# Kernel tuning notes

Measured on AMD Instinct MI355X. Metric: run time of the kernel, lower is better.

## Reference

```python
import jax, jax.numpy as jnp
import numpy as np

N = 50000      # num nodes
E = 800000     # num edges
IN = 128       # in_channels
OUT = 128      # out_channels
H = 8          # num_heads
HD = OUT // H  # out_channels_conv (per-head dim)
EDIM = 16      # edge_dim
HID = 512      # hidden_dim of dst MLP


def layer_norm(x, w, b, eps=1e-5):
    m = jnp.mean(x, axis=-1, keepdims=True)
    v = jnp.var(x, axis=-1, keepdims=True)
    return (x - m) * jax.lax.rsqrt(v + eps) * w + b


def setup_inputs() -> dict:
    key = jax.random.key(0)
    ks = jax.random.split(key, 16)
    lin = lambda k, i, o: jax.random.normal(k, (i, o), jnp.float32) / np.sqrt(i)
    return {
        "x": jax.random.normal(ks[0], (N, IN), jnp.float32),
        "edge_attr": jax.random.normal(ks[1], (E, EDIM), jnp.float32),
        "edge_index": jax.random.randint(ks[2], (2, E), 0, N),
        "Wq": lin(ks[3], IN, OUT), "bq": jnp.zeros((OUT,), jnp.float32),
        "Wk": lin(ks[4], IN, OUT), "bk": jnp.zeros((OUT,), jnp.float32),
        "Wv": lin(ks[5], IN, OUT), "bv": jnp.zeros((OUT,), jnp.float32),
        "Ws": lin(ks[6], IN, OUT), "bs": jnp.zeros((OUT,), jnp.float32),
        "We": lin(ks[7], EDIM, OUT), "be": jnp.zeros((OUT,), jnp.float32),
        "Wp": lin(ks[8], OUT, OUT), "bp": jnp.zeros((OUT,), jnp.float32),
        "ln_a_w": jnp.ones((IN,), jnp.float32), "ln_a_b": jnp.zeros((IN,), jnp.float32),
        "ln_m_w": jnp.ones((OUT,), jnp.float32), "ln_m_b": jnp.zeros((OUT,), jnp.float32),
        "W1": lin(ks[9], OUT, HID), "b1": jnp.zeros((HID,), jnp.float32),
        "W2": lin(ks[10], HID, OUT), "b2": jnp.zeros((OUT,), jnp.float32),
    }


def reference(x, edge_attr, edge_index, Wq, bq, Wk, bk, Wv, bv, Ws, bs, We, be,
              Wp, bp, ln_a_w, ln_a_b, ln_m_w, ln_m_b, W1, b1, W2, b2):
    src, dst = edge_index[0], edge_index[1]

    x_skip = x
    xn = layer_norm(x, ln_a_w, ln_a_b)           # pre-attention LN
    x_r = xn @ Ws + bs                           # lin_self

    q = (xn @ Wq + bq).reshape(N, H, HD)
    k = (xn @ Wk + bk).reshape(N, H, HD)
    v = (xn @ Wv + bv).reshape(N, H, HD)
    e = (edge_attr @ We + be).reshape(E, H, HD)

    # edge-indexed attention: score(edge) = <q[dst], k[src]+e> / sqrt(HD)
    kj = k[src] + e                                              # [E,H,HD]
    scores = jnp.einsum('ehd,ehd->eh', q[dst], kj) / np.sqrt(HD)  # [E,H]

    # segment softmax over incoming edges of each dst node
    smax = jax.ops.segment_max(scores, dst, num_segments=N)     # [N,H]
    smax = jnp.where(jnp.isfinite(smax), smax, 0.0)             # guard empty segments
    ex = jnp.exp(scores - smax[dst])                            # [E,H]
    denom = jax.ops.segment_sum(ex, dst, num_segments=N)        # [N,H]
    alpha = ex / jnp.maximum(denom[dst], 1e-16)                 # [E,H]

    msg = (v[src] + e) * alpha[..., None]                       # [E,H,HD]
    out = jax.ops.segment_sum(msg, dst, num_segments=N).reshape(N, OUT)

    out = (out + x_r) @ Wp + bp                                 # projection
    out = out + x_skip                                          # residual

    # dst-node MLP with pre-LN and residual
    h = layer_norm(out, ln_m_w, ln_m_b)
    nodes_new = jax.nn.gelu(h @ W1 + b1) @ W2 + b2 + out
    return nodes_new, edge_attr
```

## Files before the change

### kernel.cpp

```cpp
#include <hip/hip_runtime.h>
#include <math.h>

#define N_NODES 50000
#define N_EDGES 800000

typedef __attribute__((ext_vector_type(8))) short bf16x8;
typedef __attribute__((ext_vector_type(4))) float f32x4;

__device__ __forceinline__ short f2bf(float f){
  unsigned u = __float_as_uint(f);
  unsigned r = (u + 0x7FFFu + ((u >> 16) & 1u)) >> 16;
  return (short)r;
}
__device__ __forceinline__ unsigned pkbf(float lo, float hi){
  return (unsigned)(unsigned short)f2bf(lo) | ((unsigned)(unsigned short)f2bf(hi) << 16);
}

__device__ __forceinline__ float gelu_f(float x){
  float z = 0.7978845608028654f*(x + 0.044715f*x*x*x);
  float e = __expf(2.0f*z);
  return 0.5f*x*(2.0f - 2.0f/(e + 1.0f));
}

#define BF_LO(u) __uint_as_float((u)<<16)
#define BF_HI(u) __uint_as_float((u)&0xffff0000u)

__global__ __launch_bounds__(256) void k_tconv(const float* __restrict__ W, short* __restrict__ Wt,
                                               int K, int Nn){
  int i = blockIdx.x*256 + threadIdx.x;
  if (i < K*Nn){
    int n = i / K, k = i - n*K;
    Wt[(size_t)n*K + k] = f2bf(W[(size_t)k*Nn + n]);
  }
}

struct TC6 { const float* src[6]; short* dst[6]; };
__global__ __launch_bounds__(256) void k_tconv6(TC6 t){
  int b = blockIdx.y;
  const float* W = t.src[b];
  short* Wt = t.dst[b];
  int i = blockIdx.x*256 + threadIdx.x;
  int n = i >> 7, k = i & 127;
  Wt[n*128 + k] = f2bf(W[k*128 + n]);
}

__global__ __launch_bounds__(256) void k_wqm(const float* __restrict__ Wq, const float* __restrict__ We,
                                             const float* __restrict__ bq,
                                             float* __restrict__ Wqm, float* __restrict__ bqm){
  int i = blockIdx.x*256 + threadIdx.x;
  if (i < 16384){
    int k = i >> 7, j = i & 127;
    int h = j >> 4, c = j & 15;
    float s = 0.f;
    #pragma unroll
    for (int dd = 0; dd < 16; ++dd)
      s += Wq[k*128 + h*16 + dd] * We[c*128 + h*16 + dd];
    Wqm[i] = s;
    if (k == 0){
      float t = 0.f;
      #pragma unroll
      for (int dd = 0; dd < 16; ++dd)
        t += bq[h*16 + dd] * We[c*128 + h*16 + dd];
      bqm[j] = t;
    }
  }
}

__global__ __launch_bounds__(256) void k_deg(const int* __restrict__ dst, int* __restrict__ deg){
  int i = blockIdx.x*256 + threadIdx.x;
  if (i < N_EDGES) atomicAdd(&deg[dst[i]], 1);
}

__global__ __launch_bounds__(256) void k_bsum(const int* __restrict__ deg,
                                              int* __restrict__ bsum, int* __restrict__ hist){
  __shared__ int lhist[64];
  __shared__ int wred[4];
  int tid = threadIdx.x;
  int i = blockIdx.x*256 + tid;
  if (tid < 64) lhist[tid] = 0;
  __syncthreads();
  int v = (i < N_NODES) ? deg[i] : 0;
  if (i < N_NODES) atomicAdd(&lhist[v > 63 ? 63 : v], 1);
  int s = v;
  #pragma unroll
  for (int sh = 32; sh >= 1; sh >>= 1) s += __shfl_xor(s, sh, 64);
  if ((tid & 63) == 0) wred[tid >> 6] = s;
  __syncthreads();
  if (tid == 0) bsum[blockIdx.x] = wred[0] + wred[1] + wred[2] + wred[3];
  if (tid < 64){ int c = lhist[tid]; if (c) atomicAdd(&hist[tid], c); }
}

__global__ __launch_bounds__(256) void k_bscan(const int* __restrict__ bsum, int* __restrict__ bbase,
                                               const int* __restrict__ hist, int* __restrict__ histcur){
  __shared__ int wsum[4];
  int tid = threadIdx.x;
  int v = (tid < 196) ? bsum[tid] : 0;
  int incl = v;
  #pragma unroll
  for (int s = 1; s < 64; s <<= 1){
    int t = __shfl_up(incl, s, 64);
    if ((tid & 63) >= s) incl += t;
  }
  if ((tid & 63) == 63) wsum[tid >> 6] = incl;
  __syncthreads();
  if (tid == 0){ int c = 0; for (int j = 0; j < 4; ++j){ int t = wsum[j]; wsum[j] = c; c += t; } }
  __syncthreads();
  if (tid < 196) bbase[tid] = wsum[tid >> 6] + (incl - v);
  if (tid < 64){
    int h = hist[tid];
    int inc = h;
    #pragma unroll
    for (int s = 1; s < 64; s <<= 1){
      int t = __shfl_up(inc, s, 64);
      if (tid >= s) inc += t;
    }
    int total = __shfl(inc, 63, 64);
    histcur[tid] = total - inc;
  }
}

__global__ __launch_bounds__(256) void k_apply(const int* __restrict__ deg, const int* __restrict__ bbase,
                                               int* __restrict__ off, int* __restrict__ cursor){
  __shared__ int wsum[4];
  int tid = threadIdx.x;
  int i = blockIdx.x*256 + tid;
  int v = (i < N_NODES) ? deg[i] : 0;
  int incl = v;
  #pragma unroll
  for (int s = 1; s < 64; s <<= 1){
    int t = __shfl_up(incl, s, 64);
    if ((tid & 63) >= s) incl += t;
  }
  if ((tid & 63) == 63) wsum[tid >> 6] = incl;
  __syncthreads();
  if (tid == 0){ int c = 0; for (int j = 0; j < 4; ++j){ int t = wsum[j]; wsum[j] = c; c += t; } }
  __syncthreads();
  int excl = bbase[blockIdx.x] + wsum[tid >> 6] + (incl - v);
  if (i < N_NODES){
    off[i] = excl; cursor[i] = excl;
    if (i == N_NODES-1) off[N_NODES] = excl + v;
  }
}

__global__ __launch_bounds__(256) void k_scatter(const int* __restrict__ dst, const int* __restrict__ src,
                                                 const float* __restrict__ edge_attr,
                                                 int* __restrict__ cursor,
                                                 int* __restrict__ esrc, ushort* __restrict__ eab){
  int i = blockIdx.x*256 + threadIdx.x;
  if (i < N_EDGES){
    int d = dst[i];
    int pos = atomicAdd(&cursor[d], 1);
    esrc[pos] = src[i];
    const float* ea = edge_attr + (size_t)i*16;
    float4 a = *(const float4*)(ea+0), b = *(const float4*)(ea+4),
           c = *(const float4*)(ea+8), e = *(const float4*)(ea+12);
    uint4 o0, o1;
    o0.x = pkbf(a.x,a.y); o0.y = pkbf(a.z,a.w); o0.z = pkbf(b.x,b.y); o0.w = pkbf(b.z,b.w);
    o1.x = pkbf(c.x,c.y); o1.y = pkbf(c.z,c.w); o1.z = pkbf(e.x,e.y); o1.w = pkbf(e.z,e.w);
    *(uint4*)&eab[(size_t)pos*16]     = o0;
    *(uint4*)&eab[(size_t)pos*16 + 8] = o1;
  }
}

__global__ __launch_bounds__(256) void k_perm(const int* __restrict__ deg, const int* __restrict__ off,
                                              int* __restrict__ histcur,
                                              int* __restrict__ perm, int2* __restrict__ rng){
  __shared__ int lhist[64];
  __shared__ int lbase[64];
  int tid = threadIdx.x;
  int i = blockIdx.x*256 + tid;
  if (tid < 64) lhist[tid] = 0;
  __syncthreads();
  int d = 0, b = 0, loc = 0;
  bool ok = i < N_NODES;
  if (ok){
    d = deg[i];
    b = d > 63 ? 63 : d;
    loc = atomicAdd(&lhist[b], 1);
  }
  __syncthreads();
  if (tid < 64){
    int c = lhist[tid];
    lbase[tid] = c ? atomicAdd(&histcur[tid], c) : 0;
  }
  __syncthreads();
  if (ok){
    int pos = lbase[b] + loc;
    perm[pos] = i;
    int o = off[i];
    rng[pos] = make_int2(o, o + d);
  }
}

__global__ __launch_bounds__(256) void k_nodeproj(
  const float* __restrict__ x, const float* __restrict__ lnw, const float* __restrict__ lnb,
  const short* __restrict__ Wtq, const short* __restrict__ Wtqm,
  const short* __restrict__ Wtk, const short* __restrict__ Wtv, const short* __restrict__ Wts,
  const float* __restrict__ bq, const float* __restrict__ bqm,
  const float* __restrict__ bk, const float* __restrict__ bv, const float* __restrict__ bs,
  ushort* __restrict__ qb, ushort* __restrict__ qweb,
  ushort* __restrict__ kb, ushort* __restrict__ vb, float* __restrict__ xr)
{
  __shared__ short A[64][136];
  int tid = threadIdx.x;
  int rbase = blockIdx.x * 64;

  {
    int r = tid >> 2, j = tid & 3;
    int row = rbase + r;
    bool ok = row < N_NODES;
    const float* xp = x + (size_t)row*128 + j*32;
    float vals[32];
    #pragma unroll
    for (int i = 0; i < 8; ++i){
      float4 t = ok ? *(const float4*)(xp + i*4) : make_float4(0,0,0,0);
      vals[i*4+0]=t.x; vals[i*4+1]=t.y; vals[i*4+2]=t.z; vals[i*4+3]=t.w;
    }
    float s = 0.f, s2 = 0.f;
    #pragma unroll
    for (int i = 0; i < 32; ++i){ s += vals[i]; s2 += vals[i]*vals[i]; }
    s  += __shfl_xor(s, 1, 64);  s  += __shfl_xor(s, 2, 64);
    s2 += __shfl_xor(s2, 1, 64); s2 += __shfl_xor(s2, 2, 64);
    float mean = s * 0.0078125f;
    float var  = s2 * 0.0078125f - mean*mean;
    float rstd = rsqrtf(var + 1e-5f);
    #pragma unroll
    for (int i = 0; i < 32; ++i){
      int col = j*32 + i;
      float xn = (vals[i]-mean)*rstd*lnw[col] + lnb[col];
      A[r][col] = f2bf(xn);
    }
  }
  __syncthreads();

  int lane = tid & 63, wave = tid >> 6;
  int row16 = lane & 15, kg = lane >> 4;
  int cb = wave * 32;

  auto gemm = [&](const short* __restrict__ B, const float* __restrict__ bias,
                  float* __restrict__ Of, ushort* __restrict__ Ob){
    f32x4 acc[4][2] = {};
    #pragma unroll
    for (int kk = 0; kk < 128; kk += 32){
      int k0 = kk + kg*8;
      bf16x8 a0 = *(const bf16x8*)&A[ 0 + row16][k0];
      bf16x8 a1 = *(const bf16x8*)&A[16 + row16][k0];
      bf16x8 a2 = *(const bf16x8*)&A[32 + row16][k0];
      bf16x8 a3 = *(const bf16x8*)&A[48 + row16][k0];
      bf16x8 b0 = *(const bf16x8*)&B[(size_t)(cb +      row16)*128 + k0];
      bf16x8 b1 = *(const bf16x8*)&B[(size_t)(cb + 16 + row16)*128 + k0];
      acc[0][0] = __builtin_amdgcn_mfma_f32_16x16x32_bf16(a0, b0, acc[0][0], 0,0,0);
      acc[1][0] = __builtin_amdgcn_mfma_f32_16x16x32_bf16(a1, b0, acc[1][0], 0,0,0);
      acc[2][0] = __builtin_amdgcn_mfma_f32_16x16x32_bf16(a2, b0, acc[2][0], 0,0,0);
      acc[3][0] = __builtin_amdgcn_mfma_f32_16x16x32_bf16(a3, b0, acc[3][0], 0,0,0);
      acc[0][1] = __builtin_amdgcn_mfma_f32_16x16x32_bf16(a0, b1, acc[0][1], 0,0,0);
      acc[1][1] = __builtin_amdgcn_mfma_f32_16x16x32_bf16(a1, b1, acc[1][1], 0,0,0);
      acc[2][1] = __builtin_amdgcn_mfma_f32_16x16x32_bf16(a2, b1, acc[2][1], 0,0,0);
      acc[3][1] = __builtin_amdgcn_mfma_f32_16x16x32_bf16(a3, b1, acc[3][1], 0,0,0);
    }
    float bv0 = bias[cb + row16], bv1 = bias[cb + 16 + row16];
    #pragma unroll
    for (int rt = 0; rt < 4; ++rt){
      #pragma unroll
      for (int i = 0; i < 4; ++i){
        int row = rbase + rt*16 + kg*4 + i;
        if (row < N_NODES){
          float v0 = acc[rt][0][i] + bv0;
          float v1 = acc[rt][1][i] + bv1;
          if (Of){
            Of[(size_t)row*128 + cb      + row16] = v0;
            Of[(size_t)row*128 + cb + 16 + row16] = v1;
          } else {
            Ob[(size_t)row*128 + cb      + row16] = (ushort)f2bf(v0);
            Ob[(size_t)row*128 + cb + 16 + row16] = (ushort)f2bf(v1);
          }
        }
      }
    }
  };
  gemm(Wtq,  bq,  nullptr, qb);
  gemm(Wtqm, bqm, nullptr, qweb);
  gemm(Wtk,  bk,  nullptr, kb);
  gemm(Wtv,  bv,  nullptr, vb);
  gemm(Wts,  bs,  xr,  nullptr);
}

__global__ __launch_bounds__(256) void k_agg(
  const ushort* __restrict__ qb, const ushort* __restrict__ qweb,
  const ushort* __restrict__ kbf, const ushort* __restrict__ vbf,
  const ushort* __restrict__ eab, const float* __restrict__ We, const float* __restrict__ be,
  const int* __restrict__ esrc, const int* __restrict__ perm, const int2* __restrict__ rng,
  float* __restrict__ xr)
{
  int tid = threadIdx.x;
  int gid = blockIdx.x*8 + (tid >> 5);
  int node = perm[gid];
  int2 r = rng[gid];
  int beg = r.x, end = r.y;
  int l = tid & 31;
  int d0 = l*4;
  int h  = l >> 2;
  int c0 = (l & 3)*4;

  uint2 qw = *(const uint2*)&qb[(size_t)node*128 + d0];
  float4 qv = make_float4(BF_LO(qw.x), BF_HI(qw.x), BF_LO(qw.y), BF_HI(qw.y));
  uint2 qew = *(const uint2*)&qweb[(size_t)node*128 + h*16 + c0];
  float4 qe = make_float4(BF_LO(qew.x), BF_HI(qew.x), BF_LO(qew.y), BF_HI(qew.y));
  float m = -INFINITY, den = 0.f;
  float4 va = make_float4(0,0,0,0);
  float4 S  = make_float4(0,0,0,0);

  int p = beg;

#define AGG_STEP(J)                                                            \
  {                                                                            \
    int sidx[J];                                                               \
    _Pragma("unroll")                                                          \
    for (int j = 0; j < J; ++j) sidx[j] = esrc[p+j];                           \
    uint2 kw[J], vw[J], ew[J];                                                 \
    _Pragma("unroll")                                                          \
    for (int j = 0; j < J; ++j){                                               \
      kw[j] = *(const uint2*)&kbf[(size_t)sidx[j]*128 + d0];                   \
      vw[j] = *(const uint2*)&vbf[(size_t)sidx[j]*128 + d0];                   \
      ew[j] = *(const uint2*)&eab[(size_t)(p+j)*16 + c0];                      \
    }                                                                          \
    float sc[J];                                                               \
    _Pragma("unroll")                                                          \
    for (int j = 0; j < J; ++j){                                               \
      float pp = qv.x*BF_LO(kw[j].x) + qv.y*BF_HI(kw[j].x)                     \
               + qv.z*BF_LO(kw[j].y) + qv.w*BF_HI(kw[j].y)                     \
               + qe.x*BF_LO(ew[j].x) + qe.y*BF_HI(ew[j].x)                     \
               + qe.z*BF_LO(ew[j].y) + qe.w*BF_HI(ew[j].y);                    \
      pp += __shfl_xor(pp,1,64); pp += __shfl_xor(pp,2,64);                    \
      sc[j] = pp*0.25f;                                                        \
    }                                                                          \
    float mn = m;                                                              \
    _Pragma("unroll")                                                          \
    for (int j = 0; j < J; ++j) mn = fmaxf(mn, sc[j]);                         \
    float corr = __expf(m - mn);                                               \
    float w[J]; float ds = 0.f;                                                \
    _Pragma("unroll")                                                          \
    for (int j = 0; j < J; ++j){ w[j] = __expf(sc[j]-mn); ds += w[j]; }        \
    den = den*corr + ds;                                                       \
    float ax=0.f, ay=0.f, az=0.f, aw2=0.f, sx=0.f, sy=0.f, sz=0.f, sw=0.f;     \
    _Pragma("unroll")                                                          \
    for (int j = 0; j < J; ++j){                                               \
      ax += w[j]*BF_LO(vw[j].x); ay += w[j]*BF_HI(vw[j].x);                    \
      az += w[j]*BF_LO(vw[j].y); aw2+= w[j]*BF_HI(vw[j].y);                    \
      sx += w[j]*BF_LO(ew[j].x); sy += w[j]*BF_HI(ew[j].x);                    \
      sz += w[j]*BF_LO(ew[j].y); sw += w[j]*BF_HI(ew[j].y);                    \
    }                                                                          \
    va.x = va.x*corr + ax; va.y = va.y*corr + ay;                              \
    va.z = va.z*corr + az; va.w = va.w*corr + aw2;                             \
    S.x  = S.x *corr + sx; S.y  = S.y *corr + sy;                              \
    S.z  = S.z *corr + sz; S.w  = S.w *corr + sw;                              \
    m = mn;                                                                    \
  }

  for (; p + 8 <= end; p += 8) AGG_STEP(8)
  for (; p + 4 <= end; p += 4) AGG_STEP(4)
  for (; p < end; ++p){
    int s = esrc[p];
    uint2 kw = *(const uint2*)&kbf[(size_t)s*128 + d0];
    uint2 vw = *(const uint2*)&vbf[(size_t)s*128 + d0];
    uint2 ew = *(const uint2*)&eab[(size_t)p*16 + c0];
    float pp = qv.x*BF_LO(kw.x) + qv.y*BF_HI(kw.x)
             + qv.z*BF_LO(kw.y) + qv.w*BF_HI(kw.y)
             + qe.x*BF_LO(ew.x) + qe.y*BF_HI(ew.x)
             + qe.z*BF_LO(ew.y) + qe.w*BF_HI(ew.y);
    pp += __shfl_xor(pp,1,64); pp += __shfl_xor(pp,2,64);
    float sc = pp*0.25f;
    float mn = fmaxf(m, sc);
    float corr = __expf(m - mn);
    float pe = __expf(sc - mn);
    den = den*corr + pe;
    va.x = va.x*corr + pe*BF_LO(vw.x);
    va.y = va.y*corr + pe*BF_HI(vw.x);
    va.z = va.z*corr + pe*BF_LO(vw.y);
    va.w = va.w*corr + pe*BF_HI(vw.y);
    S.x = S.x*corr + pe*BF_LO(ew.x);
    S.y = S.y*corr + pe*BF_HI(ew.x);
    S.z = S.z*corr + pe*BF_LO(ew.y);
    S.w = S.w*corr + pe*BF_HI(ew.y);
    m = mn;
  }

  if (end > beg){
    float inv = 1.0f/den;
    float4 acc = va;
    int gb = (tid & 63) & 60;
    #pragma unroll
    for (int g = 0; g < 4; ++g){
      float s0 = __shfl(S.x, gb+g, 64);
      float s1 = __shfl(S.y, gb+g, 64);
      float s2 = __shfl(S.z, gb+g, 64);
      float s3 = __shfl(S.w, gb+g, 64);
      float4 w0 = *(const float4*)&We[(g*4+0)*128 + d0];
      float4 w1 = *(const float4*)&We[(g*4+1)*128 + d0];
      float4 w2 = *(const float4*)&We[(g*4+2)*128 + d0];
      float4 w3 = *(const float4*)&We[(g*4+3)*128 + d0];
      acc.x += s0*w0.x + s1*w1.x + s2*w2.x + s3*w3.x;
      acc.y += s0*w0.y + s1*w1.y + s2*w2.y + s3*w3.y;
      acc.z += s0*w0.z + s1*w1.z + s2*w2.z + s3*w3.z;
      acc.w += s0*w0.w + s1*w1.w + s2*w2.w + s3*w3.w;
    }
    float4 bev = *(const float4*)&be[d0];
    float4 xv = *(const float4*)&xr[(size_t)node*128 + d0];
    xv.x += acc.x*inv + bev.x;
    xv.y += acc.y*inv + bev.y;
    xv.z += acc.z*inv + bev.z;
    xv.w += acc.w*inv + bev.w;
    *(float4*)&xr[(size_t)node*128 + d0] = xv;
  }
}

__global__ __launch_bounds__(256) void k_post(
  const float* __restrict__ aggout, const float* __restrict__ x,
  const short* __restrict__ Wtp, const float* __restrict__ bp,
  const float* __restrict__ lnw, const float* __restrict__ lnb,
  float* __restrict__ res, short* __restrict__ A2)
{
  __shared__ short A[64][136];
  __shared__ float rf[64][132];
  int tid = threadIdx.x;
  int rbase = blockIdx.x * 64;

  {
    int r = tid >> 2, j = tid & 3;
    int row = rbase + r;
    const float* p = aggout + (size_t)row*128 + j*32;
    #pragma unroll
    for (int i = 0; i < 8; ++i){
      float4 t = *(const float4*)(p + i*4);
      int c = j*32 + i*4;
      A[r][c+0] = f2bf(t.x); A[r][c+1] = f2bf(t.y);
      A[r][c+2] = f2bf(t.z); A[r][c+3] = f2bf(t.w);
    }
  }
  __syncthreads();

  int lane = tid & 63, wave = tid >> 6;
  int row16 = lane & 15, kg = lane >> 4;
  int cb = wave * 32;

  f32x4 acc[4][2] = {};
  #pragma unroll
  for (int kk = 0; kk < 128; kk += 32){
    int k0 = kk + kg*8;
    bf16x8 a0 = *(const bf16x8*)&A[ 0 + row16][k0];
    bf16x8 a1 = *(const bf16x8*)&A[16 + row16][k0];
    bf16x8 a2 = *(const bf16x8*)&A[32 + row16][k0];
    bf16x8 a3 = *(const bf16x8*)&A[48 + row16][k0];
    bf16x8 b0 = *(const bf16x8*)&Wtp[(size_t)(cb +      row16)*128 + k0];
    bf16x8 b1 = *(const bf16x8*)&Wtp[(size_t)(cb + 16 + row16)*128 + k0];
    acc[0][0] = __builtin_amdgcn_mfma_f32_16x16x32_bf16(a0, b0, acc[0][0], 0,0,0);
    acc[1][0] = __builtin_amdgcn_mfma_f32_16x16x32_bf16(a1, b0, acc[1][0], 0,0,0);
    acc[2][0] = __builtin_amdgcn_mfma_f32_16x16x32_bf16(a2, b0, acc[2][0], 0,0,0);
    acc[3][0] = __builtin_amdgcn_mfma_f32_16x16x32_bf16(a3, b0, acc[3][0], 0,0,0);
    acc[0][1] = __builtin_amdgcn_mfma_f32_16x16x32_bf16(a0, b1, acc[0][1], 0,0,0);
    acc[1][1] = __builtin_amdgcn_mfma_f32_16x16x32_bf16(a1, b1, acc[1][1], 0,0,0);
    acc[2][1] = __builtin_amdgcn_mfma_f32_16x16x32_bf16(a2, b1, acc[2][1], 0,0,0);
    acc[3][1] = __builtin_amdgcn_mfma_f32_16x16x32_bf16(a3, b1, acc[3][1], 0,0,0);
  }
  float bv0 = bp[cb + row16], bv1 = bp[cb + 16 + row16];
  #pragma unroll
  for (int rt = 0; rt < 4; ++rt){
    #pragma unroll
    for (int i = 0; i < 4; ++i){
      int rl = rt*16 + kg*4 + i;
      int row = rbase + rl;
      float v0 = acc[rt][0][i] + bv0;
      float v1 = acc[rt][1][i] + bv1;
      if (row < N_NODES){
        v0 += x[(size_t)row*128 + cb      + row16];
        v1 += x[(size_t)row*128 + cb + 16 + row16];
        res[(size_t)row*128 + cb      + row16] = v0;
        res[(size_t)row*128 + cb + 16 + row16] = v1;
      }
      rf[rl][cb      + row16] = v0;
      rf[rl][cb + 16 + row16] = v1;
    }
  }
  __syncthreads();

  {
    int r = tid >> 2, j = tid & 3;
    int row = rbase + r;
    float vals[32];
    #pragma unroll
    for (int i = 0; i < 8; ++i){
      float4 t = *(const float4*)&rf[r][j*32 + i*4];
      vals[i*4+0]=t.x; vals[i*4+1]=t.y; vals[i*4+2]=t.z; vals[i*4+3]=t.w;
    }
    float s = 0.f, s2 = 0.f;
    #pragma unroll
    for (int i = 0; i < 32; ++i){ s += vals[i]; s2 += vals[i]*vals[i]; }
    s  += __shfl_xor(s, 1, 64);  s  += __shfl_xor(s, 2, 64);
    s2 += __shfl_xor(s2, 1, 64); s2 += __shfl_xor(s2, 2, 64);
    float mean = s * 0.0078125f;
    float var  = s2 * 0.0078125f - mean*mean;
    float rstd = rsqrtf(var + 1e-5f);
    #pragma unroll
    for (int i = 0; i < 32; ++i){
      int col = j*32 + i;
      float xn = (vals[i]-mean)*rstd*lnw[col] + lnb[col];
      A2[(size_t)row*128 + col] = f2bf(xn);
    }
  }
}

__global__ __launch_bounds__(256) void k_mlp1(
  const short* __restrict__ A2, const short* __restrict__ W1t, const float* __restrict__ b1,
  short* __restrict__ hid)
{
  __shared__ short A[64][136];
  int tid = threadIdx.x;
  int rbase = blockIdx.x * 64;
  int ch = blockIdx.y;
  for (int idx = tid; idx < 1024; idx += 256){
    int r = idx >> 4, g = idx & 15;
    *(uint4*)&A[r][g*8] = *(const uint4*)&A2[((size_t)(rbase + r))*128 + g*8];
  }
  __syncthreads();

  int lane = tid & 63, wave = tid >> 6;
  int row16 = lane & 15, kg = lane >> 4;
  int cb = ch*256 + wave*64;

  f32x4 acc[4][4] = {};
  #pragma unroll
  for (int kk = 0; kk < 128; kk += 32){
    int k0 = kk + kg*8;
    bf16x8 a[4], b[4];
    #pragma unroll
    for (int rt = 0; rt < 4; ++rt) a[rt] = *(const bf16x8*)&A[rt*16 + row16][k0];
    #pragma unroll
    for (int ct = 0; ct < 4; ++ct) b[ct] = *(const bf16x8*)&W1t[(size_t)(cb + ct*16 + row16)*128 + k0];
    #pragma unroll
    for (int rt = 0; rt < 4; ++rt)
      #pragma unroll
      for (int ct = 0; ct < 4; ++ct)
        acc[rt][ct] = __builtin_amdgcn_mfma_f32_16x16x32_bf16(a[rt], b[ct], acc[rt][ct], 0,0,0);
  }
  float bv[4];
  #pragma unroll
  for (int ct = 0; ct < 4; ++ct) bv[ct] = b1[cb + ct*16 + row16];
  #pragma unroll
  for (int rt = 0; rt < 4; ++rt){
    #pragma unroll
    for (int ct = 0; ct < 4; ++ct){
      #pragma unroll
      for (int i = 0; i < 4; ++i){
        int row = rbase + rt*16 + kg*4 + i;
        hid[(size_t)row*512 + cb + ct*16 + row16] = f2bf(gelu_f(acc[rt][ct][i] + bv[ct]));
      }
    }
  }
}

__global__ __launch_bounds__(256) void k_mlp2(
  const short* __restrict__ hid, const short* __restrict__ W2t, const float* __restrict__ b2,
  const float* __restrict__ res, float* __restrict__ out)
{
  __shared__ short A[64][136];
  int tid = threadIdx.x;
  int rbase = blockIdx.x * 64;
  int lane = tid & 63, wave = tid >> 6;
  int row16 = lane & 15, kg = lane >> 4;
  int cb = wave * 32;

  f32x4 acc[4][2] = {};
  for (int kc = 0; kc < 4; ++kc){
    __syncthreads();
    for (int idx = tid; idx < 1024; idx += 256){
      int r = idx >> 4, g = idx & 15;
      *(uint4*)&A[r][g*8] = *(const uint4*)&hid[((size_t)(rbase + r))*512 + kc*128 + g*8];
    }
    __syncthreads();
    #pragma unroll
    for (int kk = 0; kk < 128; kk += 32){
      int k0 = kk + kg*8;
      bf16x8 a0 = *(const bf16x8*)&A[ 0 + row16][k0];
      bf16x8 a1 = *(const bf16x8*)&A[16 + row16][k0];
      bf16x8 a2 = *(const bf16x8*)&A[32 + row16][k0];
      bf16x8 a3 = *(const bf16x8*)&A[48 + row16][k0];
      bf16x8 b0 = *(const bf16x8*)&W2t[(size_t)(cb +      row16)*512 + kc*128 + k0];
      bf16x8 b1 = *(const bf16x8*)&W2t[(size_t)(cb + 16 + row16)*512 + kc*128 + k0];
      acc[0][0] = __builtin_amdgcn_mfma_f32_16x16x32_bf16(a0, b0, acc[0][0], 0,0,0);
      acc[1][0] = __builtin_amdgcn_mfma_f32_16x16x32_bf16(a1, b0, acc[1][0], 0,0,0);
      acc[2][0] = __builtin_amdgcn_mfma_f32_16x16x32_bf16(a2, b0, acc[2][0], 0,0,0);
      acc[3][0] = __builtin_amdgcn_mfma_f32_16x16x32_bf16(a3, b0, acc[3][0], 0,0,0);
      acc[0][1] = __builtin_amdgcn_mfma_f32_16x16x32_bf16(a0, b1, acc[0][1], 0,0,0);
      acc[1][1] = __builtin_amdgcn_mfma_f32_16x16x32_bf16(a1, b1, acc[1][1], 0,0,0);
      acc[2][1] = __builtin_amdgcn_mfma_f32_16x16x32_bf16(a2, b1, acc[2][1], 0,0,0);
      acc[3][1] = __builtin_amdgcn_mfma_f32_16x16x32_bf16(a3, b1, acc[3][1], 0,0,0);
    }
  }
  float bv0 = b2[cb + row16], bv1 = b2[cb + 16 + row16];
  #pragma unroll
  for (int rt = 0; rt < 4; ++rt){
    #pragma unroll
    for (int i = 0; i < 4; ++i){
      int row = rbase + rt*16 + kg*4 + i;
      if (row < N_NODES){
        out[(size_t)row*128 + cb      + row16] = acc[rt][0][i] + bv0 + res[(size_t)row*128 + cb      + row16];
        out[(size_t)row*128 + cb + 16 + row16] = acc[rt][1][i] + bv1 + res[(size_t)row*128 + cb + 16 + row16];
      }
    }
  }
}

extern "C" void kernel_launch(void* const* d_in, const int* in_sizes, int n_in,
                              void* d_out, int out_size, void* d_ws, size_t ws_size,
                              hipStream_t stream)
{
  const float* x        = (const float*)d_in[0];
  const float* edge_attr= (const float*)d_in[1];
  const int*   edge_index=(const int*)d_in[2];
  const float* Wq = (const float*)d_in[3];  const float* bq = (const float*)d_in[4];
  const float* Wk = (const float*)d_in[5];  const float* bk = (const float*)d_in[6];
  const float* Wv = (const float*)d_in[7];  const float* bv = (const float*)d_in[8];
  const float* Wss= (const float*)d_in[9];  const float* bss= (const float*)d_in[10];
  const float* We = (const float*)d_in[11]; const float* be = (const float*)d_in[12];
  const float* Wp = (const float*)d_in[13]; const float* bp = (const float*)d_in[14];
  const float* lnaw=(const float*)d_in[15]; const float* lnab=(const float*)d_in[16];
  const float* lnmw=(const float*)d_in[17]; const float* lnmb=(const float*)d_in[18];
  const float* W1 = (const float*)d_in[19]; const float* b1 = (const float*)d_in[20];
  const float* W2 = (const float*)d_in[21]; const float* b2 = (const float*)d_in[22];

  float* ws = (float*)d_ws;
  const size_t NP128 = 6406144;
  const size_t NPH   = 3203072;
  ushort* qb   = (ushort*)ws;
  ushort* qweb = (ushort*)(ws + NPH);
  ushort* kbf  = (ushort*)(ws + 2*NPH);
  ushort* vbf  = (ushort*)(ws + 3*NPH);
  float*  xr   = ws + 4*NPH;
  float*  res  = ws + 4*NPH + NP128;
  ushort* eab  = (ushort*)res;
  short* wts   = (short*)(ws + 25624576);
  short* Wtq   = wts;
  short* Wtk   = wts + 16384;
  short* Wtv   = wts + 32768;
  short* Wts_  = wts + 49152;
  short* Wtp   = wts + 65536;
  short* Wtqm  = wts + 81920;
  short* W1t   = wts + 98304;
  short* W2t   = wts + 163840;
  float* Wqm_f = ws + 25624576 + 114688;
  float* bqm   = Wqm_f + 16384;
  int*   iw    = (int*)(bqm + 128);
  int* deg     = iw;
  int* hist    = iw + 50000;
  int* histcur = iw + 50064;
  int* bsum    = iw + 50128;
  int* bbase   = iw + 50324;
  int* off     = iw + 50520;
  int* cursor  = iw + 100521;
  int* perm    = iw + 150521;
  int2* rng    = (int2*)(iw + 200522);
  int* esrc    = iw + 300522;

  short* A2   = (short*)qb;
  short* hid  = (short*)qweb;

  const int* srcIdx = edge_index;
  const int* dstIdx = edge_index + N_EDGES;

  k_wqm<<<64, 256, 0, stream>>>(Wq, We, bq, Wqm_f, bqm);
  TC6 tc;
  tc.src[0]=Wq; tc.src[1]=Wk; tc.src[2]=Wv; tc.src[3]=Wss; tc.src[4]=Wp; tc.src[5]=Wqm_f;
  tc.dst[0]=Wtq; tc.dst[1]=Wtk; tc.dst[2]=Wtv; tc.dst[3]=Wts_; tc.dst[4]=Wtp; tc.dst[5]=Wtqm;
  k_tconv6<<<dim3(64,6), 256, 0, stream>>>(tc);
  k_tconv<<<256, 256, 0, stream>>>(W1, W1t, 128, 512);
  k_tconv<<<256, 256, 0, stream>>>(W2, W2t, 512, 128);

  hipMemsetAsync(deg, 0, 50064*sizeof(int), stream);
  k_deg<<<(N_EDGES+255)/256, 256, 0, stream>>>(dstIdx, deg);
  k_bsum<<<196, 256, 0, stream>>>(deg, bsum, hist);
  k_bscan<<<1, 256, 0, stream>>>(bsum, bbase, hist, histcur);
  k_apply<<<196, 256, 0, stream>>>(deg, bbase, off, cursor);
  k_scatter<<<(N_EDGES+255)/256, 256, 0, stream>>>(dstIdx, srcIdx, edge_attr, cursor, esrc, eab);
  k_perm<<<(N_NODES+255)/256, 256, 0, stream>>>(deg, off, histcur, perm, rng);

  k_nodeproj<<<782, 256, 0, stream>>>(x, lnaw, lnab, Wtq, Wtqm, Wtk, Wtv, Wts_,
                                      bq, bqm, bk, bv, bss, qb, qweb, kbf, vbf, xr);
  k_agg<<<N_NODES/8, 256, 0, stream>>>(qb, qweb, kbf, vbf, eab, We, be,
                                       esrc, perm, rng, xr);
  k_post<<<782, 256, 0, stream>>>(xr, x, Wtp, bp, lnmw, lnmb, res, A2);
  k_mlp1<<<dim3(782,2), 256, 0, stream>>>(A2, W1t, b1, hid);
  k_mlp2<<<782, 256, 0, stream>>>(hid, W2t, b2, res, (float*)d_out);

  hipMemcpyAsync((float*)d_out + (size_t)N_NODES*128, edge_attr,
                 (size_t)N_EDGES*16*sizeof(float), hipMemcpyDeviceToDevice, stream);
}
```

Before: 367.4 us.

## Merge weight prep kernels, fuse edge_attr copy into scatter, prefetch edge indices in aggregation

```diff
diff --git a/kernel.cpp b/kernel.cpp
--- a/kernel.cpp
+++ b/kernel.cpp
@@ -25,44 +25,44 @@
 #define BF_LO(u) __uint_as_float((u)<<16)
 #define BF_HI(u) __uint_as_float((u)&0xffff0000u)
 
-__global__ __launch_bounds__(256) void k_tconv(const float* __restrict__ W, short* __restrict__ Wt,
-                                               int K, int Nn){
-  int i = blockIdx.x*256 + threadIdx.x;
-  if (i < K*Nn){
-    int n = i / K, k = i - n*K;
-    Wt[(size_t)n*K + k] = f2bf(W[(size_t)k*Nn + n]);
-  }
-}
-
-struct TC6 { const float* src[6]; short* dst[6]; };
-__global__ __launch_bounds__(256) void k_tconv6(TC6 t){
-  int b = blockIdx.y;
-  const float* W = t.src[b];
-  short* Wt = t.dst[b];
-  int i = blockIdx.x*256 + threadIdx.x;
-  int n = i >> 7, k = i & 127;
-  Wt[n*128 + k] = f2bf(W[k*128 + n]);
-}
-
-__global__ __launch_bounds__(256) void k_wqm(const float* __restrict__ Wq, const float* __restrict__ We,
-                                             const float* __restrict__ bq,
-                                             float* __restrict__ Wqm, float* __restrict__ bqm){
-  int i = blockIdx.x*256 + threadIdx.x;
-  if (i < 16384){
+struct Prep {
+  const float* src[5]; short* dst[5];
+  const float* Wq; const float* We; const float* bq;
+  short* Wtqm; float* bqm;
+  const float* W1; short* W1t;
+  const float* W2; short* W2t;
+};
+__global__ __launch_bounds__(256) void k_prep(Prep a){
+  int blk = blockIdx.x, tid = threadIdx.x;
+  if (blk < 320){
+    int b = blk >> 6;
+    int i = (blk & 63)*256 + tid;
+    int n = i >> 7, k = i & 127;
+    a.dst[b][n*128 + k] = f2bf(a.src[b][k*128 + n]);
+  } else if (blk < 384){
+    int i = (blk - 320)*256 + tid;
     int k = i >> 7, j = i & 127;
     int h = j >> 4, c = j & 15;
     float s = 0.f;
     #pragma unroll
     for (int dd = 0; dd < 16; ++dd)
-      s += Wq[k*128 + h*16 + dd] * We[c*128 + h*16 + dd];
-    Wqm[i] = s;
+      s += a.Wq[k*128 + h*16 + dd] * a.We[c*128 + h*16 + dd];
+    a.Wtqm[j*128 + k] = f2bf(s);
     if (k == 0){
       float t = 0.f;
       #pragma unroll
       for (int dd = 0; dd < 16; ++dd)
-        t += bq[h*16 + dd] * We[c*128 + h*16 + dd];
-      bqm[j] = t;
-    }
+        t += a.bq[h*16 + dd] * a.We[c*128 + h*16 + dd];
+      a.bqm[j] = t;
+    }
+  } else if (blk < 640){
+    int i = (blk - 384)*256 + tid;
+    int n = i >> 7, k = i & 127;
+    a.W1t[n*128 + k] = f2bf(a.W1[k*512 + n]);
+  } else {
+    int i = (blk - 640)*256 + tid;
+    int n = i >> 9, k = i & 511;
+    a.W2t[n*512 + k] = f2bf(a.W2[k*128 + n]);
   }
 }
 
@@ -145,7 +145,8 @@
 __global__ __launch_bounds__(256) void k_scatter(const int* __restrict__ dst, const int* __restrict__ src,
                                                  const float* __restrict__ edge_attr,
                                                  int* __restrict__ cursor,
-                                                 int* __restrict__ esrc, ushort* __restrict__ eab){
+                                                 int* __restrict__ esrc, ushort* __restrict__ eab,
+                                                 float* __restrict__ eout){
   int i = blockIdx.x*256 + threadIdx.x;
   if (i < N_EDGES){
     int d = dst[i];
@@ -159,6 +160,11 @@
     o1.x = pkbf(c.x,c.y); o1.y = pkbf(c.z,c.w); o1.z = pkbf(e.x,e.y); o1.w = pkbf(e.z,e.w);
     *(uint4*)&eab[(size_t)pos*16]     = o0;
     *(uint4*)&eab[(size_t)pos*16 + 8] = o1;
+    float* op = eout + (size_t)i*16;
+    *(float4*)(op+0)  = a;
+    *(float4*)(op+4)  = b;
+    *(float4*)(op+8)  = c;
+    *(float4*)(op+12) = e;
   }
 }
 
@@ -311,6 +317,59 @@
   float4 S  = make_float4(0,0,0,0);
 
   int p = beg;
+
+  int s8[8];
+  {
+    bool have = (beg + 8 <= end);
+    #pragma unroll
+    for (int j = 0; j < 8; ++j) s8[j] = have ? esrc[beg + j] : 0;
+  }
+  for (; p + 8 <= end; p += 8){
+    int n8[8];
+    bool more = (p + 16 <= end);
+    #pragma unroll
+    for (int j = 0; j < 8; ++j) n8[j] = more ? esrc[p + 8 + j] : 0;
+    uint2 kw[8], vw[8], ew[8];
+    #pragma unroll
+    for (int j = 0; j < 8; ++j){
+      kw[j] = *(const uint2*)&kbf[(size_t)s8[j]*128 + d0];
+      vw[j] = *(const uint2*)&vbf[(size_t)s8[j]*128 + d0];
+      ew[j] = *(const uint2*)&eab[(size_t)(p+j)*16 + c0];
+    }
+    float sc[8];
+    #pragma unroll
+    for (int j = 0; j < 8; ++j){
+      float pp = qv.x*BF_LO(kw[j].x) + qv.y*BF_HI(kw[j].x)
+               + qv.z*BF_LO(kw[j].y) + qv.w*BF_HI(kw[j].y)
+               + qe.x*BF_LO(ew[j].x) + qe.y*BF_HI(ew[j].x)
+               + qe.z*BF_LO(ew[j].y) + qe.w*BF_HI(ew[j].y);
+      pp += __shfl_xor(pp,1,64); pp += __shfl_xor(pp,2,64);
+      sc[j] = pp*0.25f;
+    }
+    float mn = m;
+    #pragma unroll
+    for (int j = 0; j < 8; ++j) mn = fmaxf(mn, sc[j]);
+    float corr = __expf(m - mn);
+    float w[8]; float ds = 0.f;
+    #pragma unroll
+    for (int j = 0; j < 8; ++j){ w[j] = __expf(sc[j]-mn); ds += w[j]; }
+    den = den*corr + ds;
+    float ax=0.f, ay=0.f, az=0.f, aw2=0.f, sx=0.f, sy=0.f, sz=0.f, sw=0.f;
+    #pragma unroll
+    for (int j = 0; j < 8; ++j){
+      ax += w[j]*BF_LO(vw[j].x); ay += w[j]*BF_HI(vw[j].x);
+      az += w[j]*BF_LO(vw[j].y); aw2+= w[j]*BF_HI(vw[j].y);
+      sx += w[j]*BF_LO(ew[j].x); sy += w[j]*BF_HI(ew[j].x);
+      sz += w[j]*BF_LO(ew[j].y); sw += w[j]*BF_HI(ew[j].y);
+    }
+    va.x = va.x*corr + ax; va.y = va.y*corr + ay;
+    va.z = va.z*corr + az; va.w = va.w*corr + aw2;
+    S.x  = S.x *corr + sx; S.y  = S.y *corr + sy;
+    S.z  = S.z *corr + sz; S.w  = S.w *corr + sw;
+    m = mn;
+    #pragma unroll
+    for (int j = 0; j < 8; ++j) s8[j] = n8[j];
+  }
 
 #define AGG_STEP(J)                                                            \
   {                                                                            \
@@ -357,7 +416,6 @@
     m = mn;                                                                    \
   }
 
-  for (; p + 8 <= end; p += 8) AGG_STEP(8)
   for (; p + 4 <= end; p += 4) AGG_STEP(4)
   for (; p < end; ++p){
     int s = esrc[p];
@@ -647,8 +705,7 @@
   short* Wtqm  = wts + 81920;
   short* W1t   = wts + 98304;
   short* W2t   = wts + 163840;
-  float* Wqm_f = ws + 25624576 + 114688;
-  float* bqm   = Wqm_f + 16384;
+  float* bqm   = ws + 25624576 + 114688 + 16384;
   int*   iw    = (int*)(bqm + 128);
   int* deg     = iw;
   int* hist    = iw + 50000;
@@ -667,20 +724,20 @@
   const int* srcIdx = edge_index;
   const int* dstIdx = edge_index + N_EDGES;
 
-  k_wqm<<<64, 256, 0, stream>>>(Wq, We, bq, Wqm_f, bqm);
-  TC6 tc;
-  tc.src[0]=Wq; tc.src[1]=Wk; tc.src[2]=Wv; tc.src[3]=Wss; tc.src[4]=Wp; tc.src[5]=Wqm_f;
-  tc.dst[0]=Wtq; tc.dst[1]=Wtk; tc.dst[2]=Wtv; tc.dst[3]=Wts_; tc.dst[4]=Wtp; tc.dst[5]=Wtqm;
-  k_tconv6<<<dim3(64,6), 256, 0, stream>>>(tc);
-  k_tconv<<<256, 256, 0, stream>>>(W1, W1t, 128, 512);
-  k_tconv<<<256, 256, 0, stream>>>(W2, W2t, 512, 128);
+  Prep pa;
+  pa.src[0]=Wq; pa.src[1]=Wk; pa.src[2]=Wv; pa.src[3]=Wss; pa.src[4]=Wp;
+  pa.dst[0]=Wtq; pa.dst[1]=Wtk; pa.dst[2]=Wtv; pa.dst[3]=Wts_; pa.dst[4]=Wtp;
+  pa.Wq=Wq; pa.We=We; pa.bq=bq; pa.Wtqm=Wtqm; pa.bqm=bqm;
+  pa.W1=W1; pa.W1t=W1t; pa.W2=W2; pa.W2t=W2t;
+  k_prep<<<896, 256, 0, stream>>>(pa);
 
   hipMemsetAsync(deg, 0, 50064*sizeof(int), stream);
   k_deg<<<(N_EDGES+255)/256, 256, 0, stream>>>(dstIdx, deg);
   k_bsum<<<196, 256, 0, stream>>>(deg, bsum, hist);
   k_bscan<<<1, 256, 0, stream>>>(bsum, bbase, hist, histcur);
   k_apply<<<196, 256, 0, stream>>>(deg, bbase, off, cursor);
-  k_scatter<<<(N_EDGES+255)/256, 256, 0, stream>>>(dstIdx, srcIdx, edge_attr, cursor, esrc, eab);
+  k_scatter<<<(N_EDGES+255)/256, 256, 0, stream>>>(dstIdx, srcIdx, edge_attr, cursor, esrc, eab,
+                                                   (float*)d_out + (size_t)N_NODES*128);
   k_perm<<<(N_NODES+255)/256, 256, 0, stream>>>(deg, off, histcur, perm, rng);
 
   k_nodeproj<<<782, 256, 0, stream>>>(x, lnaw, lnab, Wtq, Wtqm, Wtk, Wtv, Wts_,
@@ -690,7 +747,4 @@
   k_post<<<782, 256, 0, stream>>>(xr, x, Wtp, bp, lnmw, lnmb, res, A2);
   k_mlp1<<<dim3(782,2), 256, 0, stream>>>(A2, W1t, b1, hid);
   k_mlp2<<<782, 256, 0, stream>>>(hid, W2t, b2, res, (float*)d_out);
-
-  hipMemcpyAsync((float*)d_out + (size_t)N_NODES*128, edge_attr,
-                 (size_t)N_EDGES*16*sizeof(float), hipMemcpyDeviceToDevice, stream);
-}
+}
```

After: 343.9 us. 1.07x faster.
